# Kernel tuning notes

Hardware: AMD Instinct MI355X
Metric: run time of the kernel (lower is better)

Reference implementation:

```python
import jax, jax.numpy as jnp
import numpy as np

B, N, D = 16, 1369, 1024
HID, NH = 512, 8
SCALE = np.sqrt(D // NH)


def _pos_encoding_2d(n, d):
    ps = int(np.sqrt(n))  # 37; n is a perfect square here
    div = jnp.exp(jnp.arange(0, d // 2, 2, dtype=jnp.float32) * (-np.log(10000.0) / (d // 2)))
    rows = (jnp.arange(n) // ps).astype(jnp.float32)
    cols = (jnp.arange(n) % ps).astype(jnp.float32)
    def interleave(s, c):
        return jnp.stack([s, c], axis=-1).reshape(n, -1)
    half_row = interleave(jnp.sin(rows[:, None] * div), jnp.cos(rows[:, None] * div))
    half_col = interleave(jnp.sin(cols[:, None] * div), jnp.cos(cols[:, None] * div))
    return jnp.concatenate([half_row, half_col], axis=-1)  # [n, d]


def _center_bias(n, strength=0.3):
    ps = int(np.sqrt(n))
    c = ps // 2
    y, x = jnp.meshgrid(jnp.arange(ps, dtype=jnp.float32), jnp.arange(ps, dtype=jnp.float32), indexing='ij')
    d2 = (x - c) ** 2 + (y - c) ** 2
    sigma = ps / 6.0
    return (jnp.exp(-d2 / (2.0 * sigma ** 2)).reshape(-1)) * strength  # [n]


def setup_inputs() -> dict:
    key = jax.random.key(0)
    ks = jax.random.split(key, 16)
    s = 0.02
    return {
        'patch_tokens': jax.random.normal(ks[0], (B, N, D), dtype=jnp.float32),
        'curiosity_score': jax.random.uniform(ks[1], (B,), dtype=jnp.float32),
        'Wq': jax.random.normal(ks[2], (D, D), dtype=jnp.float32) * s,
        'bq': jax.random.uniform(ks[3], (D,), minval=-0.05, maxval=0.05, dtype=jnp.float32),
        'Wk': jax.random.normal(ks[4], (D, D), dtype=jnp.float32) * s,
        'bk': jax.random.uniform(ks[5], (D,), minval=-0.05, maxval=0.05, dtype=jnp.float32),
        'Wv': jax.random.normal(ks[6], (D, D), dtype=jnp.float32) * s,
        'bv': jnp.zeros((D,), dtype=jnp.float32),
        'Wc1': jax.random.normal(ks[7], (1, HID // 8), dtype=jnp.float32) * s,
        'bc1': jnp.zeros((HID // 8,), dtype=jnp.float32),
        'Wc2': jax.random.normal(ks[8], (HID // 8, NH), dtype=jnp.float32) * s,
        'bc2': jnp.zeros((NH,), dtype=jnp.float32),
        'Wp1': jax.random.normal(ks[9], (D, HID), dtype=jnp.float32) * s,
        'bp1': jnp.zeros((HID,), dtype=jnp.float32),
        'Wp2': jax.random.normal(ks[10], (HID, HID // 4), dtype=jnp.float32) * s,
        'bp2': jnp.zeros((HID // 4,), dtype=jnp.float32),
        'adaptive_weight': jnp.float32(0.5),
    }


def reference(patch_tokens, curiosity_score, Wq, bq, Wk, bk, Wv, bv,
              Wc1, bc1, Wc2, bc2, Wp1, bp1, Wp2, bp2, adaptive_weight):
    b, n, d = patch_tokens.shape
    x = patch_tokens + _pos_encoding_2d(n, d)[None]  # [B,N,D]

    q = x @ Wq + bq
    k = x @ Wk + bk
    v = x @ Wv + bv

    scores = jnp.einsum('bqd,bkd->bqk', q, k) / SCALE          # [B,N,N]
    attn = jax.nn.softmax(scores, axis=-1)                     # dropout p=0 / eval
    attended = jnp.einsum('bqk,bkd->bqd', attn, v)             # [B,N,D]

    cb = _center_bias(n)[None]                                 # [1,N]
    VAR_EPS = 1e-6

    pa = attn.mean(axis=1) + cb
    # fallback chain (data-dependent in torch; expressed with jnp.where)
    pa2 = jnp.diagonal(attn, axis1=-2, axis2=-1) + cb
    pa = jnp.where(jnp.var(pa, ddof=1) < VAR_EPS, pa2, pa)
    pa3 = attn.max(axis=-1) + cb
    pa = jnp.where(jnp.var(pa, ddof=1) < VAR_EPS, pa3, pa)
    norms = jnp.linalg.norm(x, axis=-1)
    noise = jax.random.normal(jax.random.key(42), norms.shape, dtype=norms.dtype) * 0.1 * jnp.std(norms, ddof=1)
    pa = jnp.where(jnp.var(pa, ddof=1) < VAR_EPS, norms + noise, pa)

    pa = pa / (pa.sum(axis=-1, keepdims=True) + 1e-8)

    # curiosity modulation
    h = jax.nn.relu(curiosity_score[:, None] @ Wc1 + bc1)
    cm = jax.nn.sigmoid(h @ Wc2 + bc2)                         # [B,NH]
    cw = cm.mean(axis=-1, keepdims=True)                       # [B,1]
    modulated = pa * (1.0 + cw)
    fa = adaptive_weight * modulated + (1.0 - adaptive_weight) * pa

    fa = jnp.clip(fa, 1e-8, None)
    fa = fa / (fa.sum(axis=-1, keepdims=True) + 1e-8)

    weighted = jnp.sum(attended * fa[..., None], axis=1)       # [B,D]
    focal = jax.nn.relu(weighted @ Wp1 + bp1) @ Wp2 + bp2      # [B,HID//4]
    return focal, fa
```

## Files before the change

### kernel.cpp

```cpp
#include <hip/hip_runtime.h>
#include <hip/hip_bf16.h>
#include <cstdint>

#define B_   16
#define N_   1369
#define NP   1536
#define D_   1024
#define NQKV 3072
#define SLD  1568
#define QLD  3104

typedef __bf16 bf16x8_t __attribute__((ext_vector_type(8)));
typedef __bf16 bf16x4_t __attribute__((ext_vector_type(4)));
typedef float  f32x4_t  __attribute__((ext_vector_type(4)));

__device__ __forceinline__ float  bf2f(__bf16 x) { return (float)x; }
__device__ __forceinline__ __bf16 f2bf(float x)  { return (__bf16)x; }

#define GLOAD_LDS16(g, l) __builtin_amdgcn_global_load_lds( \
    (const __attribute__((address_space(1))) void*)(g),     \
    (__attribute__((address_space(3))) void*)(l), 16, 0, 0)

__global__ __launch_bounds__(256)
void pos_kernel(float* __restrict__ pos)
{
    const int idx = blockIdx.x * 256 + threadIdx.x;
    if (idx >= N_ * D_) return;
    const int n = idx >> 10, f = idx & 1023;
    const int row = n / 37, col = n - row * 37;
    const float base = (f < 512) ? (float)row : (float)col;
    const int  t2   = (f & 511) >> 1;
    const float dv  = __expf(-0.03597789207803197f * (float)t2);
    const float ang = base * dv;
    pos[idx] = (f & 1) ? cosf(ang) : sinf(ang);
}

__global__ __launch_bounds__(256)
void addpos_kernel(const float* __restrict__ patch, const float* __restrict__ pos,
                   __bf16* __restrict__ X)
{
    const long tid = (long)blockIdx.x * 256 + threadIdx.x;
    const long e   = tid * 4;
    const int  f   = (int)(e & 1023);
    const long nb  = e >> 10;
    const int  n   = (int)(nb % NP);
    const long b   = nb / NP;
    bf16x4_t o;
    if (n < N_) {
        const float4 p = *(const float4*)(patch + ((b * N_ + n) << 10) + f);
        const float4 q = *(const float4*)(pos + ((long)n << 10) + f);
        o[0] = f2bf(p.x + q.x); o[1] = f2bf(p.y + q.y);
        o[2] = f2bf(p.z + q.z); o[3] = f2bf(p.w + q.w);
    } else {
        o[0] = o[1] = o[2] = o[3] = f2bf(0.f);
    }
    *(bf16x4_t*)(X + e) = o;
}

__global__ __launch_bounds__(256)
void wcast_kernel(const float* __restrict__ W0, const float* __restrict__ W1,
                  const float* __restrict__ W2,
                  __bf16* __restrict__ T0, __bf16* __restrict__ T1, __bf16* __restrict__ T2)
{
    const float* W = blockIdx.z == 0 ? W0 : (blockIdx.z == 1 ? W1 : W2);
    __bf16*      T = blockIdx.z == 0 ? T0 : (blockIdx.z == 1 ? T1 : T2);
    __shared__ float tile[64][65];
    const int o0 = blockIdx.x * 64, i0 = blockIdx.y * 64;
    const int t = threadIdx.x;
    const int tr = t >> 4, tc = (t & 15) * 4;
    #pragma unroll
    for (int rr = 0; rr < 64; rr += 16) {
        float4 v = *(const float4*)(W + (long)(i0 + rr + tr) * 1024 + o0 + tc);
        tile[rr + tr][tc + 0] = v.x; tile[rr + tr][tc + 1] = v.y;
        tile[rr + tr][tc + 2] = v.z; tile[rr + tr][tc + 3] = v.w;
    }
    __syncthreads();
    #pragma unroll
    for (int rr = 0; rr < 64; rr += 16) {
        bf16x4_t o;
        o[0] = f2bf(tile[tc + 0][rr + tr]); o[1] = f2bf(tile[tc + 1][rr + tr]);
        o[2] = f2bf(tile[tc + 2][rr + tr]); o[3] = f2bf(tile[tc + 3][rr + tr]);
        *(bf16x4_t*)(T + (long)(o0 + rr + tr) * 1024 + i0 + tc) = o;
    }
}

__global__ __launch_bounds__(256)
void bcat_kernel(const float* __restrict__ bq, const float* __restrict__ bk,
                 const float* __restrict__ bv, float* __restrict__ bcat)
{
    const int i = blockIdx.x * 256 + threadIdx.x;
    if (i >= NQKV) return;
    const int p = i >> 10, j = i & 1023;
    bcat[i] = p == 0 ? bq[j] : (p == 1 ? bk[j] : bv[j]);
}

template<int HAS_BIAS>
__global__ __launch_bounds__(512, 2)
void gemm256(const __bf16* __restrict__ A, const __bf16* __restrict__ Bt,
             __bf16* __restrict__ C, const float* __restrict__ bias,
             int lda, int ldb, int ldc, int Kd, float scale,
             long sA, long sB, long sC, int tilesN, int tilesPerBatch, int cpx)
{
    __shared__ __bf16 lds[65536];
    const int bid = blockIdx.x;
    const int vt  = (bid & 7) * cpx + (bid >> 3);
    const int bz  = vt / tilesPerBatch;
    const int rem = vt - bz * tilesPerBatch;
    const int ty  = rem / tilesN;
    const int tx  = rem - ty * tilesN;
    A  += (long)bz * sA;  Bt += (long)bz * sB;  C += (long)bz * sC;
    const int m0 = ty * 256, n0 = tx * 256;

    const int t  = threadIdx.x;
    const int w  = t >> 6, l = t & 63;
    const int wr = w >> 2, wc = w & 3;
    const int lr = l & 15, lh = l >> 4;

    const int laneF  = (lr * 64 + ((lh * 16) ^ (((lr >> 3) & 1) << 5))) >> 1;
    const int rstage = w * 16 + (l >> 2);
    const int kstage = ((l & 3) * 8) ^ (((l >> 5) & 1) << 4);

    const __bf16* Ag = A  + (long)(m0 + rstage) * lda + kstage;
    const __bf16* Bg = Bt + (long)(n0 + rstage) * ldb + kstage;
    __bf16* dA = lds + w * 1024;
    __bf16* dB = lds + 16384 + w * 1024;

#define SA_(buf, half, kt) do {                                       \
    const __bf16* g_ = Ag + (long)(half) * 128 * lda + (kt) * 64;     \
    __bf16* d_ = dA + (buf) * 32768 + (half) * 8192;                  \
    GLOAD_LDS16(g_, d_); GLOAD_LDS16(g_ + 32, d_ + 512); } while (0)
#define SB_(buf, half, kt) do {                                       \
    const __bf16* g_ = Bg + (long)(half) * 128 * ldb + (kt) * 64;     \
    __bf16* d_ = dB + (buf) * 32768 + (half) * 8192;                  \
    GLOAD_LDS16(g_, d_); GLOAD_LDS16(g_ + 32, d_ + 512); } while (0)

    f32x4_t acc[8][4] = {};

    const int NT = Kd >> 6;
    SA_(0, 0, 0); SA_(0, 1, 0); SB_(0, 0, 0); SB_(0, 1, 0);
    asm volatile("s_waitcnt vmcnt(0)" ::: "memory");
    __builtin_amdgcn_s_barrier();

    for (int tk = 0; tk < NT; ++tk) {
        const int c = tk & 1, o = c ^ 1;
        const int cbase = c * 32768;
        if (tk + 1 < NT) {
            SA_(o, 0, tk + 1); SA_(o, 1, tk + 1);
            SB_(o, 0, tk + 1); SB_(o, 1, tk + 1);
        }
        const __bf16* bp = lds + cbase + 16384 + wc * 4096 + laneF;
        const __bf16* ap = lds + cbase + wr * 8192 + laneF;
        bf16x8_t bf0[4], bf1[4], af0[8], af1[8];
        #pragma unroll
        for (int nn = 0; nn < 4; ++nn) bf0[nn] = *(const bf16x8_t*)(bp + nn * 1024);
        #pragma unroll
        for (int mi = 0; mi < 8; ++mi) af0[mi] = *(const bf16x8_t*)(ap + mi * 1024);
        #pragma unroll
        for (int nn = 0; nn < 4; ++nn) bf1[nn] = *(const bf16x8_t*)(bp + nn * 1024 + 512);
        #pragma unroll
        for (int mi = 0; mi < 8; ++mi) af1[mi] = *(const bf16x8_t*)(ap + mi * 1024 + 512);
        __builtin_amdgcn_s_setprio(1);
        #pragma unroll
        for (int mi = 0; mi < 8; ++mi)
            #pragma unroll
            for (int nn = 0; nn < 4; ++nn)
                acc[mi][nn] = __builtin_amdgcn_mfma_f32_16x16x32_bf16(af0[mi], bf0[nn], acc[mi][nn], 0, 0, 0);
        #pragma unroll
        for (int mi = 0; mi < 8; ++mi)
            #pragma unroll
            for (int nn = 0; nn < 4; ++nn)
                acc[mi][nn] = __builtin_amdgcn_mfma_f32_16x16x32_bf16(af1[mi], bf1[nn], acc[mi][nn], 0, 0, 0);
        __builtin_amdgcn_s_setprio(0);
        asm volatile("s_waitcnt vmcnt(0)" ::: "memory");
        __builtin_amdgcn_s_barrier();
    }

    #pragma unroll
    for (int mi = 0; mi < 8; ++mi) {
        const int row = m0 + wr * 128 + mi * 16 + lh * 4;
        #pragma unroll
        for (int nn = 0; nn < 4; ++nn) {
            const int col = n0 + wc * 64 + nn * 16 + lr;
            const float bb = HAS_BIAS ? bias[col] : 0.0f;
            #pragma unroll
            for (int q = 0; q < 4; ++q)
                C[(long)(row + q) * ldc + col] = f2bf(acc[mi][nn][q] * scale + bb);
        }
    }
#undef SA_
#undef SB_
}

__global__ __launch_bounds__(256)
void softmax_kernel(__bf16* __restrict__ S)
{
    const int wid  = threadIdx.x >> 6;
    const int lane = threadIdx.x & 63;
    const int q    = blockIdx.x * 4 + wid;
    const int b    = blockIdx.y;
    if (q >= N_) return;
    __bf16* row = S + ((long)b * NP + q) * SLD;
    float v[24];
    float m = -1e30f;
    #pragma unroll
    for (int j = 0; j < 3; ++j) {
        const int k0 = j * 512 + lane * 8;
        bf16x8_t raw = *(const bf16x8_t*)(row + k0);
        #pragma unroll
        for (int i = 0; i < 8; ++i) {
            const float x = (k0 + i < N_) ? bf2f(raw[i]) : -1e30f;
            v[j * 8 + i] = x; m = fmaxf(m, x);
        }
    }
    #pragma unroll
    for (int o = 32; o; o >>= 1) m = fmaxf(m, __shfl_xor(m, o));
    float s = 0.f;
    #pragma unroll
    for (int j = 0; j < 3; ++j) {
        const int k0 = j * 512 + lane * 8;
        #pragma unroll
        for (int i = 0; i < 8; ++i) {
            if (k0 + i < N_) { const float e = __expf(v[j * 8 + i] - m); v[j * 8 + i] = e; s += e; }
            else             v[j * 8 + i] = 0.f;
        }
    }
    #pragma unroll
    for (int o = 32; o; o >>= 1) s += __shfl_xor(s, o);
    const float inv = 1.f / s;
    #pragma unroll
    for (int j = 0; j < 3; ++j) {
        const int k0 = j * 512 + lane * 8;
        bf16x8_t o8;
        #pragma unroll
        for (int i = 0; i < 8; ++i) o8[i] = f2bf(v[j * 8 + i] * inv);
        *(bf16x8_t*)(row + k0) = o8;
    }
}

template<int WEIGHTED>
__global__ __launch_bounds__(256)
void colsum_kernel(const __bf16* __restrict__ attn, const float* __restrict__ wv,
                   float* __restrict__ out)
{
    const int t = threadIdx.x;
    if (t >= 192) return;
    const int b  = blockIdx.y;
    const int q0 = blockIdx.x * 16;
    const int q1 = (q0 + 16 < N_) ? q0 + 16 : N_;
    const int k8 = t * 8;
    float s[8] = {};
    const __bf16* base = attn + (long)b * NP * SLD + k8;
    for (int q = q0; q < q1; ++q) {
        bf16x8_t v = *(const bf16x8_t*)(base + (long)q * SLD);
        const float wq = WEIGHTED ? wv[b * NP + q] : 1.0f;
        #pragma unroll
        for (int i = 0; i < 8; ++i) s[i] += wq * bf2f(v[i]);
    }
    #pragma unroll
    for (int i = 0; i < 8; ++i) atomicAdd(out + b * NP + k8 + i, s[i]);
}

__global__ __launch_bounds__(256)
void fa_kernel(const float* __restrict__ pa_raw, const float* __restrict__ curiosity,
               const float* __restrict__ Wc1, const float* __restrict__ bc1,
               const float* __restrict__ Wc2, const float* __restrict__ bc2,
               const float* __restrict__ aw_p,
               float* __restrict__ fa_ws, float* __restrict__ out_fa)
{
    const int b = blockIdx.x, t = threadIdx.x;
    __shared__ float hsh[64];
    __shared__ float red[8];
    __shared__ float cwsh;
    if (t < 64) hsh[t] = fmaxf(0.f, curiosity[b] * Wc1[t] + bc1[t]);
    __syncthreads();
    if (t < 8) {
        float a = bc2[t];
        for (int j = 0; j < 64; ++j) a += hsh[j] * Wc2[j * 8 + t];
        red[t] = 1.f / (1.f + __expf(-a));
    }
    __syncthreads();
    if (t == 0) {
        float cw = 0.f;
        for (int i = 0; i < 8; ++i) cw += red[i];
        cwsh = cw * 0.125f;
    }
    __syncthreads();
    const float aw   = aw_p[0];
    const float modf = 1.f + aw * cwsh;
    const float sig  = 37.f / 6.f;
    const float inv2s2 = 1.f / (2.f * sig * sig);
    float pv[6];
    float s1 = 0.f;
    #pragma unroll
    for (int i = 0; i < 6; ++i) {
        const int k = t + i * 256;
        float p = 0.f;
        if (k < N_) {
            const int y = k / 37, x = k - y * 37;
            const float d2 = (float)((x - 18) * (x - 18) + (y - 18) * (y - 18));
            const float cb = 0.3f * __expf(-d2 * inv2s2);
            p = pa_raw[b * NP + k] * (1.f / 1369.f) + cb;
        }
        pv[i] = p; s1 += p;
    }
    #pragma unroll
    for (int o = 32; o; o >>= 1) s1 += __shfl_xor(s1, o);
    __syncthreads();
    if (!(t & 63)) red[t >> 6] = s1;
    __syncthreads();
    s1 = red[0] + red[1] + red[2] + red[3];
    const float inv1 = 1.f / (s1 + 1e-8f);
    float s2 = 0.f;
    #pragma unroll
    for (int i = 0; i < 6; ++i) {
        const int k = t + i * 256;
        if (k < N_) {
            const float f = fmaxf(pv[i] * inv1 * modf, 1e-8f);
            pv[i] = f; s2 += f;
        }
    }
    #pragma unroll
    for (int o = 32; o; o >>= 1) s2 += __shfl_xor(s2, o);
    if (!(t & 63)) red[4 + (t >> 6)] = s2;
    __syncthreads();
    s2 = red[4] + red[5] + red[6] + red[7];
    const float inv2 = 1.f / (s2 + 1e-8f);
    #pragma unroll
    for (int i = 0; i < 6; ++i) {
        const int k = t + i * 256;
        if (k < N_) {
            const float f = pv[i] * inv2;
            fa_ws[b * NP + k]  = f;
            out_fa[b * N_ + k] = f;
        }
    }
}

__global__ __launch_bounds__(256)
void weighted_kernel(const float* __restrict__ g, const __bf16* __restrict__ V,
                     int ldv, float* __restrict__ wout)
{
    const int b  = blockIdx.y;
    const int k0 = blockIdx.x * 86;
    const int k1 = (k0 + 86 < N_) ? k0 + 86 : N_;
    const int d  = threadIdx.x * 4;
    float a0 = 0, a1 = 0, a2 = 0, a3 = 0;
    const __bf16* vb = V + (long)b * NP * ldv + d;
    for (int k = k0; k < k1; ++k) {
        const float gv = g[b * NP + k];
        bf16x4_t vv = *(const bf16x4_t*)(vb + (long)k * ldv);
        a0 += gv * bf2f(vv[0]); a1 += gv * bf2f(vv[1]);
        a2 += gv * bf2f(vv[2]); a3 += gv * bf2f(vv[3]);
    }
    atomicAdd(wout + b * D_ + d + 0, a0);
    atomicAdd(wout + b * D_ + d + 1, a1);
    atomicAdd(wout + b * D_ + d + 2, a2);
    atomicAdd(wout + b * D_ + d + 3, a3);
}

__global__ __launch_bounds__(256)
void focal1_kernel(const float* __restrict__ weighted, const float* __restrict__ Wp1,
                   const float* __restrict__ bp1, float* __restrict__ h)
{
    const int b = blockIdx.y, jc = blockIdx.x;
    const int t = threadIdx.x;
    const int jl = t >> 2, part = t & 3;
    const int j = jc * 64 + jl;
    const float* wb = weighted + b * 1024 + part * 256;
    const float* wp = Wp1 + (long)(part * 256) * 512 + j;
    float a = 0.f;
    #pragma unroll 8
    for (int d = 0; d < 256; ++d) a += wb[d] * wp[(long)d * 512];
    a += __shfl_xor(a, 1);
    a += __shfl_xor(a, 2);
    if (part == 0) h[b * 512 + j] = fmaxf(a + bp1[j], 0.f);
}

__global__ __launch_bounds__(128)
void focal2_kernel(const float* __restrict__ h, const float* __restrict__ Wp2,
                   const float* __restrict__ bp2, float* __restrict__ out)
{
    const int b = blockIdx.x, o = threadIdx.x;
    __shared__ float hs[512];
    for (int i = o; i < 512; i += 128) hs[i] = h[b * 512 + i];
    __syncthreads();
    float a = bp2[o];
    #pragma unroll 8
    for (int j = 0; j < 512; ++j) a += hs[j] * Wp2[j * 128 + o];
    out[b * 128 + o] = a;
}

extern "C" void kernel_launch(void* const* d_in, const int* in_sizes, int n_in,
                              void* d_out, int out_size, void* d_ws, size_t ws_size,
                              hipStream_t stream)
{
    const float* patch     = (const float*)d_in[0];
    const float* curiosity = (const float*)d_in[1];
    const float* Wq  = (const float*)d_in[2];
    const float* bq  = (const float*)d_in[3];
    const float* Wk  = (const float*)d_in[4];
    const float* bk  = (const float*)d_in[5];
    const float* Wv  = (const float*)d_in[6];
    const float* bv  = (const float*)d_in[7];
    const float* Wc1 = (const float*)d_in[8];
    const float* bc1 = (const float*)d_in[9];
    const float* Wc2 = (const float*)d_in[10];
    const float* bc2 = (const float*)d_in[11];
    const float* Wp1 = (const float*)d_in[12];
    const float* bp1 = (const float*)d_in[13];
    const float* Wp2 = (const float*)d_in[14];
    const float* bp2 = (const float*)d_in[15];
    const float* aw  = (const float*)d_in[16];
    float* out = (float*)d_out;

    char* ws = (char*)d_ws;
    size_t off = 0;
    auto alloc = [&](size_t bytes) -> char* {
        char* p = ws + off;
        off += (bytes + 255) & ~(size_t)255;
        return p;
    };
    float*  pos  = (float*) alloc((size_t)N_ * D_ * 4);
    __bf16* X    = (__bf16*)alloc((size_t)B_ * NP * D_ * 2);
    __bf16* WT   = (__bf16*)alloc((size_t)3 * D_ * D_ * 2);
    const size_t S_BYTES = (size_t)B_ * NP * SLD * 2;
    if (off < S_BYTES) off = S_BYTES;
    __bf16* S    = (__bf16*)ws;
    __bf16* QKV  = (__bf16*)alloc((size_t)B_ * NP * QLD * 2);
    float*  pa   = (float*) alloc((size_t)B_ * NP * 4);
    float*  faw  = (float*) alloc((size_t)B_ * NP * 4);
    float*  gbuf = (float*) alloc((size_t)B_ * NP * 4);
    float*  wsum = (float*) alloc((size_t)B_ * D_ * 4);
    float*  bcat = (float*) alloc((size_t)NQKV * 4);
    float*  hbuf = (float*) alloc((size_t)B_ * 512 * 4);

    (void)hipMemsetAsync(pa,   0, (size_t)B_ * NP * 4, stream);
    (void)hipMemsetAsync(gbuf, 0, (size_t)B_ * NP * 4, stream);
    (void)hipMemsetAsync(wsum, 0, (size_t)B_ * D_ * 4, stream);

    pos_kernel<<<(N_ * D_ + 255) / 256, 256, 0, stream>>>(pos);
    addpos_kernel<<<(int)((size_t)B_ * NP * D_ / 4 / 256), 256, 0, stream>>>(patch, pos, X);
    {
        dim3 g(16, 16, 3);
        wcast_kernel<<<g, 256, 0, stream>>>(Wq, Wk, Wv,
                                            WT, WT + D_ * D_, WT + 2 * D_ * D_);
    }
    bcat_kernel<<<(NQKV + 255) / 256, 256, 0, stream>>>(bq, bk, bv, bcat);
    {
        const int nwg = 96 * 12;
        gemm256<1><<<nwg, 512, 0, stream>>>(X, WT, QKV, bcat,
                                            D_, D_, QLD, D_, 1.0f,
                                            0, 0, 0, 12, nwg, nwg / 8);
    }
    {
        const int nwg = 36 * B_;
        gemm256<0><<<nwg, 512, 0, stream>>>(QKV, QKV + D_, S, nullptr,
                                            QLD, QLD, SLD, D_,
                                            0.08838834764831845f,
                                            (long)NP * QLD, (long)NP * QLD,
                                            (long)NP * SLD, 6, 36, nwg / 8);
    }
    {
        dim3 g((N_ + 3) / 4, B_);
        softmax_kernel<<<g, 256, 0, stream>>>(S);
    }
    {
        dim3 g(86, B_);
        colsum_kernel<0><<<g, 256, 0, stream>>>(S, nullptr, pa);
    }
    fa_kernel<<<B_, 256, 0, stream>>>(pa, curiosity, Wc1, bc1, Wc2, bc2, aw,
                                      faw, out + B_ * 128);
    {
        dim3 g(86, B_);
        colsum_kernel<1><<<g, 256, 0, stream>>>(S, faw, gbuf);
    }
    {
        dim3 g(16, B_);
        weighted_kernel<<<g, 256, 0, stream>>>(gbuf, QKV + 2 * D_, QLD, wsum);
    }
    {
        dim3 g(8, B_);
        focal1_kernel<<<g, 256, 0, stream>>>(wsum, Wp1, bp1, hbuf);
    }
    focal2_kernel<<<B_, 128, 0, stream>>>(hbuf, Wp2, bp2, out);
}
```

Measured before the change: 560.4 us.

## Fuse softmax row statistics into score GEMM epilogue and widen GEMM to 1024 threads

Removes the standalone softmax pass. The score GEMM epilogue now computes per-tile row max and sum-exp, a small combine kernel merges the partials, and the column-sum kernels apply exp(s-M)/Z on the fly to the raw scores. Both GEMMs also move from 512 to 1024 threads per block with a 4x4 accumulator tile per wave, halving per-thread register use. The cost is a recomputed exp in both colsum passes and extra epilogue reductions, and the attention values are exponentiated from bf16-rounded scores rather than stored normalized.

```diff
diff --git a/kernel.cpp b/kernel.cpp
--- a/kernel.cpp
+++ b/kernel.cpp
@@ -94,10 +94,11 @@
     bcat[i] = p == 0 ? bq[j] : (p == 1 ? bk[j] : bv[j]);
 }
 
-template<int HAS_BIAS>
-__global__ __launch_bounds__(512, 2)
+template<int HAS_BIAS, int STATS>
+__global__ __launch_bounds__(1024, 4)
 void gemm256(const __bf16* __restrict__ A, const __bf16* __restrict__ Bt,
              __bf16* __restrict__ C, const float* __restrict__ bias,
+             float2* __restrict__ mzp,
              int lda, int ldb, int ldc, int Kd, float scale,
              long sA, long sB, long sC, int tilesN, int tilesPerBatch, int cpx)
 {
@@ -117,24 +118,20 @@
     const int lr = l & 15, lh = l >> 4;
 
     const int laneF  = (lr * 64 + ((lh * 16) ^ (((lr >> 3) & 1) << 5))) >> 1;
-    const int rstage = w * 16 + (l >> 2);
-    const int kstage = ((l & 3) * 8) ^ (((l >> 5) & 1) << 4);
+    const int rstage = (w >> 1) * 16 + (l >> 2);
+    const int kstage = (w & 1) * 32 + (((l & 3) * 8) ^ (((l >> 5) & 1) << 4));
 
     const __bf16* Ag = A  + (long)(m0 + rstage) * lda + kstage;
     const __bf16* Bg = Bt + (long)(n0 + rstage) * ldb + kstage;
-    __bf16* dA = lds + w * 1024;
-    __bf16* dB = lds + 16384 + w * 1024;
-
-#define SA_(buf, half, kt) do {                                       \
-    const __bf16* g_ = Ag + (long)(half) * 128 * lda + (kt) * 64;     \
-    __bf16* d_ = dA + (buf) * 32768 + (half) * 8192;                  \
-    GLOAD_LDS16(g_, d_); GLOAD_LDS16(g_ + 32, d_ + 512); } while (0)
-#define SB_(buf, half, kt) do {                                       \
-    const __bf16* g_ = Bg + (long)(half) * 128 * ldb + (kt) * 64;     \
-    __bf16* d_ = dB + (buf) * 32768 + (half) * 8192;                  \
-    GLOAD_LDS16(g_, d_); GLOAD_LDS16(g_ + 32, d_ + 512); } while (0)
-
-    f32x4_t acc[8][4] = {};
+    __bf16* dA = lds + w * 512;
+    __bf16* dB = lds + 16384 + w * 512;
+
+#define SA_(buf, half, kt) GLOAD_LDS16(Ag + (long)(half) * 128 * lda + (kt) * 64, \
+                                       dA + (buf) * 32768 + (half) * 8192)
+#define SB_(buf, half, kt) GLOAD_LDS16(Bg + (long)(half) * 128 * ldb + (kt) * 64, \
+                                       dB + (buf) * 32768 + (half) * 8192)
+
+    f32x4_t acc[4][4] = {};
 
     const int NT = Kd >> 6;
     SA_(0, 0, 0); SA_(0, 1, 0); SB_(0, 0, 0); SB_(0, 1, 0);
@@ -143,41 +140,43 @@
 
     for (int tk = 0; tk < NT; ++tk) {
         const int c = tk & 1, o = c ^ 1;
-        const int cbase = c * 32768;
         if (tk + 1 < NT) {
             SA_(o, 0, tk + 1); SA_(o, 1, tk + 1);
             SB_(o, 0, tk + 1); SB_(o, 1, tk + 1);
         }
-        const __bf16* bp = lds + cbase + 16384 + wc * 4096 + laneF;
-        const __bf16* ap = lds + cbase + wr * 8192 + laneF;
-        bf16x8_t bf0[4], bf1[4], af0[8], af1[8];
-        #pragma unroll
-        for (int nn = 0; nn < 4; ++nn) bf0[nn] = *(const bf16x8_t*)(bp + nn * 1024);
-        #pragma unroll
-        for (int mi = 0; mi < 8; ++mi) af0[mi] = *(const bf16x8_t*)(ap + mi * 1024);
-        #pragma unroll
-        for (int nn = 0; nn < 4; ++nn) bf1[nn] = *(const bf16x8_t*)(bp + nn * 1024 + 512);
-        #pragma unroll
-        for (int mi = 0; mi < 8; ++mi) af1[mi] = *(const bf16x8_t*)(ap + mi * 1024 + 512);
+        const int cb = c * 32768;
+        const __bf16* ap = lds + cb + (wr >> 1) * 8192 + (wr & 1) * 4096 + laneF;
+        const __bf16* bp = lds + cb + 16384 + (wc >> 1) * 8192 + (wc & 1) * 4096 + laneF;
+        bf16x8_t af[4], bfm[4];
+        #pragma unroll
+        for (int nn = 0; nn < 4; ++nn) bfm[nn] = *(const bf16x8_t*)(bp + nn * 1024);
+        #pragma unroll
+        for (int mi = 0; mi < 4; ++mi) af[mi]  = *(const bf16x8_t*)(ap + mi * 1024);
         __builtin_amdgcn_s_setprio(1);
         #pragma unroll
-        for (int mi = 0; mi < 8; ++mi)
+        for (int mi = 0; mi < 4; ++mi)
             #pragma unroll
             for (int nn = 0; nn < 4; ++nn)
-                acc[mi][nn] = __builtin_amdgcn_mfma_f32_16x16x32_bf16(af0[mi], bf0[nn], acc[mi][nn], 0, 0, 0);
-        #pragma unroll
-        for (int mi = 0; mi < 8; ++mi)
+                acc[mi][nn] = __builtin_amdgcn_mfma_f32_16x16x32_bf16(af[mi], bfm[nn], acc[mi][nn], 0, 0, 0);
+        __builtin_amdgcn_s_setprio(0);
+        #pragma unroll
+        for (int nn = 0; nn < 4; ++nn) bfm[nn] = *(const bf16x8_t*)(bp + nn * 1024 + 512);
+        #pragma unroll
+        for (int mi = 0; mi < 4; ++mi) af[mi]  = *(const bf16x8_t*)(ap + mi * 1024 + 512);
+        __builtin_amdgcn_s_setprio(1);
+        #pragma unroll
+        for (int mi = 0; mi < 4; ++mi)
             #pragma unroll
             for (int nn = 0; nn < 4; ++nn)
-                acc[mi][nn] = __builtin_amdgcn_mfma_f32_16x16x32_bf16(af1[mi], bf1[nn], acc[mi][nn], 0, 0, 0);
+                acc[mi][nn] = __builtin_amdgcn_mfma_f32_16x16x32_bf16(af[mi], bfm[nn], acc[mi][nn], 0, 0, 0);
         __builtin_amdgcn_s_setprio(0);
         asm volatile("s_waitcnt vmcnt(0)" ::: "memory");
         __builtin_amdgcn_s_barrier();
     }
 
     #pragma unroll
-    for (int mi = 0; mi < 8; ++mi) {
-        const int row = m0 + wr * 128 + mi * 16 + lh * 4;
+    for (int mi = 0; mi < 4; ++mi) {
+        const int row = m0 + wr * 64 + mi * 16 + lh * 4;
         #pragma unroll
         for (int nn = 0; nn < 4; ++nn) {
             const int col = n0 + wc * 64 + nn * 16 + lr;
@@ -187,60 +186,71 @@
                 C[(long)(row + q) * ldc + col] = f2bf(acc[mi][nn][q] * scale + bb);
         }
     }
+
+    if (STATS) {
+        __syncthreads();
+        float* lm = (float*)lds;
+        float* lz = lm + 1024;
+        #pragma unroll
+        for (int mi = 0; mi < 4; ++mi) {
+            #pragma unroll
+            for (int qq = 0; qq < 4; ++qq) {
+                float vb[4]; float m = -3.0e38f;
+                #pragma unroll
+                for (int nn = 0; nn < 4; ++nn) {
+                    const int col = n0 + wc * 64 + nn * 16 + lr;
+                    const float vr = bf2f(f2bf(acc[mi][nn][qq] * scale));
+                    vb[nn] = (col < N_) ? vr : -3.0e38f;
+                    m = fmaxf(m, vb[nn]);
+                }
+                #pragma unroll
+                for (int o = 1; o <= 8; o <<= 1) m = fmaxf(m, __shfl_xor(m, o));
+                float z = 0.f;
+                #pragma unroll
+                for (int nn = 0; nn < 4; ++nn) z += __expf(vb[nn] - m);
+                #pragma unroll
+                for (int o = 1; o <= 8; o <<= 1) z += __shfl_xor(z, o);
+                if (lr == 0) {
+                    const int r = wr * 64 + mi * 16 + lh * 4 + qq;
+                    lm[r * 4 + wc] = m; lz[r * 4 + wc] = z;
+                }
+            }
+        }
+        __syncthreads();
+        if (t < 256) {
+            const float ma = lm[t * 4 + 0], mb = lm[t * 4 + 1];
+            const float mc = lm[t * 4 + 2], md = lm[t * 4 + 3];
+            const float M = fmaxf(fmaxf(ma, mb), fmaxf(mc, md));
+            const float Z = lz[t * 4 + 0] * __expf(ma - M) + lz[t * 4 + 1] * __expf(mb - M)
+                          + lz[t * 4 + 2] * __expf(mc - M) + lz[t * 4 + 3] * __expf(md - M);
+            mzp[((long)bz * NP + ty * 256 + t) * 6 + tx] = make_float2(M, Z);
+        }
+    }
 #undef SA_
 #undef SB_
 }
 
 __global__ __launch_bounds__(256)
-void softmax_kernel(__bf16* __restrict__ S)
-{
-    const int wid  = threadIdx.x >> 6;
-    const int lane = threadIdx.x & 63;
-    const int q    = blockIdx.x * 4 + wid;
-    const int b    = blockIdx.y;
-    if (q >= N_) return;
-    __bf16* row = S + ((long)b * NP + q) * SLD;
-    float v[24];
-    float m = -1e30f;
-    #pragma unroll
-    for (int j = 0; j < 3; ++j) {
-        const int k0 = j * 512 + lane * 8;
-        bf16x8_t raw = *(const bf16x8_t*)(row + k0);
-        #pragma unroll
-        for (int i = 0; i < 8; ++i) {
-            const float x = (k0 + i < N_) ? bf2f(raw[i]) : -1e30f;
-            v[j * 8 + i] = x; m = fmaxf(m, x);
-        }
-    }
-    #pragma unroll
-    for (int o = 32; o; o >>= 1) m = fmaxf(m, __shfl_xor(m, o));
-    float s = 0.f;
-    #pragma unroll
-    for (int j = 0; j < 3; ++j) {
-        const int k0 = j * 512 + lane * 8;
-        #pragma unroll
-        for (int i = 0; i < 8; ++i) {
-            if (k0 + i < N_) { const float e = __expf(v[j * 8 + i] - m); v[j * 8 + i] = e; s += e; }
-            else             v[j * 8 + i] = 0.f;
-        }
-    }
-    #pragma unroll
-    for (int o = 32; o; o >>= 1) s += __shfl_xor(s, o);
-    const float inv = 1.f / s;
-    #pragma unroll
-    for (int j = 0; j < 3; ++j) {
-        const int k0 = j * 512 + lane * 8;
-        bf16x8_t o8;
-        #pragma unroll
-        for (int i = 0; i < 8; ++i) o8[i] = f2bf(v[j * 8 + i] * inv);
-        *(bf16x8_t*)(row + k0) = o8;
-    }
+void combine_kernel(const float2* __restrict__ mzp,
+                    float* __restrict__ rowM, float* __restrict__ rowZi)
+{
+    const int i = blockIdx.x * 256 + threadIdx.x;
+    if (i >= B_ * NP) return;
+    float2 p[6]; float M = -3.0e38f;
+    #pragma unroll
+    for (int k = 0; k < 6; ++k) { p[k] = mzp[(long)i * 6 + k]; M = fmaxf(M, p[k].x); }
+    float Z = 0.f;
+    #pragma unroll
+    for (int k = 0; k < 6; ++k) Z += p[k].y * __expf(p[k].x - M);
+    rowM[i]  = M;
+    rowZi[i] = 1.f / Z;
 }
 
 template<int WEIGHTED>
 __global__ __launch_bounds__(256)
-void colsum_kernel(const __bf16* __restrict__ attn, const float* __restrict__ wv,
-                   float* __restrict__ out)
+void colsum_kernel(const __bf16* __restrict__ attn,
+                   const float* __restrict__ rowM, const float* __restrict__ rowZi,
+                   const float* __restrict__ wv, float* __restrict__ out)
 {
     const int t = threadIdx.x;
     if (t >= 192) return;
@@ -252,9 +262,11 @@
     const __bf16* base = attn + (long)b * NP * SLD + k8;
     for (int q = q0; q < q1; ++q) {
         bf16x8_t v = *(const bf16x8_t*)(base + (long)q * SLD);
-        const float wq = WEIGHTED ? wv[b * NP + q] : 1.0f;
-        #pragma unroll
-        for (int i = 0; i < 8; ++i) s[i] += wq * bf2f(v[i]);
+        const float Mq = rowM[b * NP + q];
+        float wq = rowZi[b * NP + q];
+        if (WEIGHTED) wq *= wv[b * NP + q];
+        #pragma unroll
+        for (int i = 0; i < 8; ++i) s[i] += wq * __expf(bf2f(v[i]) - Mq);
     }
     #pragma unroll
     for (int i = 0; i < 8; ++i) atomicAdd(out + b * NP + k8 + i, s[i]);
@@ -433,6 +445,9 @@
     float*  wsum = (float*) alloc((size_t)B_ * D_ * 4);
     float*  bcat = (float*) alloc((size_t)NQKV * 4);
     float*  hbuf = (float*) alloc((size_t)B_ * 512 * 4);
+    float2* mzp  = (float2*)alloc((size_t)B_ * NP * 6 * 8);
+    float*  rowM = (float*) alloc((size_t)B_ * NP * 4);
+    float*  rowZi= (float*) alloc((size_t)B_ * NP * 4);
 
     (void)hipMemsetAsync(pa,   0, (size_t)B_ * NP * 4, stream);
     (void)hipMemsetAsync(gbuf, 0, (size_t)B_ * NP * 4, stream);
@@ -448,31 +463,28 @@
     bcat_kernel<<<(NQKV + 255) / 256, 256, 0, stream>>>(bq, bk, bv, bcat);
     {
         const int nwg = 96 * 12;
-        gemm256<1><<<nwg, 512, 0, stream>>>(X, WT, QKV, bcat,
-                                            D_, D_, QLD, D_, 1.0f,
-                                            0, 0, 0, 12, nwg, nwg / 8);
+        gemm256<1, 0><<<nwg, 1024, 0, stream>>>(X, WT, QKV, bcat, nullptr,
+                                                D_, D_, QLD, D_, 1.0f,
+                                                0, 0, 0, 12, nwg, nwg / 8);
     }
     {
         const int nwg = 36 * B_;
-        gemm256<0><<<nwg, 512, 0, stream>>>(QKV, QKV + D_, S, nullptr,
-                                            QLD, QLD, SLD, D_,
-                                            0.08838834764831845f,
-                                            (long)NP * QLD, (long)NP * QLD,
-                                            (long)NP * SLD, 6, 36, nwg / 8);
-    }
-    {
-        dim3 g((N_ + 3) / 4, B_);
-        softmax_kernel<<<g, 256, 0, stream>>>(S);
-    }
+        gemm256<0, 1><<<nwg, 1024, 0, stream>>>(QKV, QKV + D_, S, nullptr, mzp,
+                                                QLD, QLD, SLD, D_,
+                                                0.08838834764831845f,
+                                                (long)NP * QLD, (long)NP * QLD,
+                                                (long)NP * SLD, 6, 36, nwg / 8);
+    }
+    combine_kernel<<<(B_ * NP + 255) / 256, 256, 0, stream>>>(mzp, rowM, rowZi);
     {
         dim3 g(86, B_);
-        colsum_kernel<0><<<g, 256, 0, stream>>>(S, nullptr, pa);
+        colsum_kernel<0><<<g, 256, 0, stream>>>(S, rowM, rowZi, nullptr, pa);
     }
     fa_kernel<<<B_, 256, 0, stream>>>(pa, curiosity, Wc1, bc1, Wc2, bc2, aw,
                                       faw, out + B_ * 128);
     {
         dim3 g(86, B_);
-        colsum_kernel<1><<<g, 256, 0, stream>>>(S, faw, gbuf);
+        colsum_kernel<1><<<g, 256, 0, stream>>>(S, rowM, rowZi, faw, gbuf);
     }
     {
         dim3 g(16, B_);
```

Measured after the change: 552.7 us. No clear change (-1.4%).
